# Kernel tuning notes

Measured on AMD Instinct MI355X. Metric: run time of the kernel, lower is better.

## Reference

```python
import jax, jax.numpy as jnp
import numpy as np

ALPHA = 1.0


def _bce_with_logits(x, y):
    # torch BCEWithLogitsLoss (mean): y*softplus(-x) + (1-y)*softplus(x)
    return jnp.mean(y * jax.nn.softplus(-x) + (1.0 - y) * jax.nn.softplus(x))


def _cross_entropy(logits, labels):
    # torch CrossEntropyLoss (mean) with int class labels
    logp = jax.nn.log_softmax(logits, axis=-1)
    return -jnp.mean(jnp.take_along_axis(logp, labels[:, None], axis=-1))


def setup_inputs() -> dict:
    key = jax.random.key(0)
    ks = jax.random.split(key, 6)
    B, T, C = 2097152, 4, 16
    return {
        "y_pred_binary": jax.random.normal(ks[0], (B,), dtype=jnp.float32),
        "y_pred_type": jax.random.normal(ks[1], (B, T), dtype=jnp.float32),
        "y_pred_source": jax.random.normal(ks[2], (B, C), dtype=jnp.float32),
        "y_true_binary": jnp.round(jax.random.uniform(ks[3], (B,), dtype=jnp.float32)),
        "y_true_type": jnp.round(jax.random.uniform(ks[4], (B, T), dtype=jnp.float32)),
        "y_true_source": jax.random.randint(ks[5], (B,), 0, C, dtype=jnp.int32),
    }


def reference(y_pred_binary, y_pred_type, y_pred_source,
              y_true_binary, y_true_type, y_true_source):
    loss = _bce_with_logits(y_pred_binary, y_true_binary)
    loss = loss + _bce_with_logits(y_pred_type, y_true_type)
    loss = loss + _cross_entropy(y_pred_source, y_true_source)

    # Non-differentiable consistency counts (torch computes these under
    # no_grad / via round+argmax, which carry no gradient).
    pb = jax.lax.stop_gradient(y_pred_binary)
    pt = jax.lax.stop_gradient(y_pred_type)
    ps = jax.lax.stop_gradient(y_pred_source)

    binary_c = jax.nn.sigmoid(pb) >= 0.5                     # [B] bool (round(sigmoid))
    type_c = jnp.any(jax.nn.sigmoid(pt) >= 0.5, axis=1)      # [B] bool
    source_c = jnp.argmax(ps, axis=1) > 0                    # [B] bool

    # XOR: exactly one of the pair active -> inconsistent
    cons_ab = jnp.mean((binary_c ^ type_c).astype(jnp.float32))
    cons_ac = jnp.mean((binary_c ^ source_c).astype(jnp.float32))

    loss = loss + ALPHA * cons_ab + ALPHA * cons_ac
    return loss
```

## Files before the change

kernel.cpp:

```cpp
#include <hip/hip_runtime.h>
#include <math.h>

#define CPB 4
#define ROWS_PER_BLOCK (256 * CPB)

__device__ __forceinline__ float fast_softplus(float x) {
    return fmaxf(x, 0.0f) + __logf(1.0f + __expf(-fabsf(x)));
}

struct Row {
    float  xb, yb;
    int    lab;
    float4 xt, yt;
    float4 r0, r1, r2, r3;
};

__device__ __forceinline__ Row load_row(const float* __restrict__ pb,
                                        const float* __restrict__ tb,
                                        const int*   __restrict__ ts,
                                        const float4* __restrict__ pt4,
                                        const float4* __restrict__ tt4,
                                        const float4* __restrict__ ps4,
                                        int row)
{
    Row R;
    R.xb  = pb[row];
    R.yb  = tb[row];
    R.lab = ts[row];
    R.xt  = pt4[row];
    R.yt  = tt4[row];
    size_t b = (size_t)row * 4;
    R.r0 = ps4[b + 0];
    R.r1 = ps4[b + 1];
    R.r2 = ps4[b + 2];
    R.r3 = ps4[b + 3];
    return R;
}

__device__ __forceinline__ float row_contrib(const Row& R)
{
    float c = fast_softplus(R.xb) - R.yb * R.xb;
    bool bin_c = (R.xb >= 0.0f);

    float tsum = (fast_softplus(R.xt.x) - R.yt.x * R.xt.x)
               + (fast_softplus(R.xt.y) - R.yt.y * R.xt.y)
               + (fast_softplus(R.xt.z) - R.yt.z * R.xt.z)
               + (fast_softplus(R.xt.w) - R.yt.w * R.xt.w);
    c += 0.25f * tsum;
    bool type_c = (R.xt.x >= 0.0f) || (R.xt.y >= 0.0f) ||
                  (R.xt.z >= 0.0f) || (R.xt.w >= 0.0f);

    float v[16] = { R.r0.x, R.r0.y, R.r0.z, R.r0.w,
                    R.r1.x, R.r1.y, R.r1.z, R.r1.w,
                    R.r2.x, R.r2.y, R.r2.z, R.r2.w,
                    R.r3.x, R.r3.y, R.r3.z, R.r3.w };
    float m = v[0];
    #pragma unroll
    for (int j = 1; j < 16; ++j) m = fmaxf(m, v[j]);
    float s = 0.0f;
    #pragma unroll
    for (int j = 0; j < 16; ++j) s += __expf(v[j] - m);
    float vlab = v[0];
    #pragma unroll
    for (int j = 1; j < 16; ++j) vlab = (R.lab == j) ? v[j] : vlab;
    c += m + __logf(s) - vlab;

    float mr = v[1];
    #pragma unroll
    for (int j = 2; j < 16; ++j) mr = fmaxf(mr, v[j]);
    bool src_c = (mr > v[0]);

    c += (bin_c != type_c) ? 1.0f : 0.0f;
    c += (bin_c != src_c)  ? 1.0f : 0.0f;
    return c;
}

__global__ __launch_bounds__(256, 2) void multitask_loss_kernel(
    const float*  __restrict__ pb,
    const float4* __restrict__ pt4,
    const float4* __restrict__ ps4,
    const float*  __restrict__ tb,
    const float4* __restrict__ tt4,
    const int*    __restrict__ ts,
    float*        __restrict__ partials)
{
    const int tid = threadIdx.x;
    const int row0 = blockIdx.x * ROWS_PER_BLOCK + tid;

    float acc = 0.0f;
    Row cur = load_row(pb, tb, ts, pt4, tt4, ps4, row0);
    #pragma unroll
    for (int i = 0; i < CPB - 1; ++i) {
        Row nxt = load_row(pb, tb, ts, pt4, tt4, ps4, row0 + (i + 1) * 256);
        acc += row_contrib(cur);
        cur = nxt;
    }
    acc += row_contrib(cur);

    #pragma unroll
    for (int off = 32; off > 0; off >>= 1)
        acc += __shfl_down(acc, off, 64);

    __shared__ float wsum[4];
    const int lane = tid & 63;
    const int wave = tid >> 6;
    if (lane == 0) wsum[wave] = acc;
    __syncthreads();
    if (tid == 0)
        partials[blockIdx.x] = wsum[0] + wsum[1] + wsum[2] + wsum[3];
}

__global__ __launch_bounds__(256) void reduce_kernel(
    const float* __restrict__ partials, int nblocks,
    const float*  __restrict__ pb,
    const float4* __restrict__ pt4,
    const float4* __restrict__ ps4,
    const float*  __restrict__ tb,
    const float4* __restrict__ tt4,
    const int*    __restrict__ ts,
    int n_main, int B,
    float* __restrict__ out, double invB)
{
    double s = 0.0;
    for (int i = threadIdx.x; i < nblocks; i += 256)
        s += (double)partials[i];
    for (int r = n_main + threadIdx.x; r < B; r += 256)
        s += (double)row_contrib(load_row(pb, tb, ts, pt4, tt4, ps4, r));

    #pragma unroll
    for (int off = 32; off > 0; off >>= 1)
        s += __shfl_down(s, off, 64);

    __shared__ double wsum[4];
    int lane = threadIdx.x & 63;
    int wave = threadIdx.x >> 6;
    if (lane == 0) wsum[wave] = s;
    __syncthreads();
    if (threadIdx.x == 0)
        out[0] = (float)((wsum[0] + wsum[1] + wsum[2] + wsum[3]) * invB);
}

extern "C" void kernel_launch(void* const* d_in, const int* in_sizes, int n_in,
                              void* d_out, int out_size, void* d_ws, size_t ws_size,
                              hipStream_t stream) {
    const float*  pb  = (const float*)d_in[0];
    const float4* pt4 = (const float4*)d_in[1];
    const float4* ps4 = (const float4*)d_in[2];
    const float*  tb  = (const float*)d_in[3];
    const float4* tt4 = (const float4*)d_in[4];
    const int*    ts  = (const int*)d_in[5];
    int B = in_sizes[0];

    float* partials = (float*)d_ws;

    int grid   = B / ROWS_PER_BLOCK;
    int n_main = grid * ROWS_PER_BLOCK;

    multitask_loss_kernel<<<grid, 256, 0, stream>>>(pb, pt4, ps4, tb, tt4, ts,
                                                    partials);
    reduce_kernel<<<1, 256, 0, stream>>>(partials, grid,
                                         pb, pt4, ps4, tb, tt4, ts,
                                         n_main, B, (float*)d_out,
                                         1.0 / (double)B);
}
```

Before: 265.9 us.

## Fold softplus/logsumexp logs into products, one row per thread, ballot penalties

```diff
diff --git a/kernel.cpp b/kernel.cpp
--- a/kernel.cpp
+++ b/kernel.cpp
@@ -1,110 +1,119 @@
 #include <hip/hip_runtime.h>
 #include <math.h>
 
-#define CPB 4
-#define ROWS_PER_BLOCK (256 * CPB)
+#define L2E 1.44269504088896340736f
+#define LN2 0.69314718055994530942f
 
-__device__ __forceinline__ float fast_softplus(float x) {
-    return fmaxf(x, 0.0f) + __logf(1.0f + __expf(-fabsf(x)));
-}
+#if __has_builtin(__builtin_amdgcn_exp2f)
+__device__ __forceinline__ float fexp2(float x)  { return __builtin_amdgcn_exp2f(x); }
+#else
+__device__ __forceinline__ float fexp2(float x)  { return __exp2f(x); }
+#endif
+#if __has_builtin(__builtin_amdgcn_logf)
+__device__ __forceinline__ float flog2(float x)  { return __builtin_amdgcn_logf(x); }
+#else
+__device__ __forceinline__ float flog2(float x)  { return __log2f(x); }
+#endif
 
-struct Row {
-    float  xb, yb;
-    int    lab;
-    float4 xt, yt;
-    float4 r0, r1, r2, r3;
-};
-
-__device__ __forceinline__ Row load_row(const float* __restrict__ pb,
-                                        const float* __restrict__ tb,
-                                        const int*   __restrict__ ts,
-                                        const float4* __restrict__ pt4,
-                                        const float4* __restrict__ tt4,
-                                        const float4* __restrict__ ps4,
-                                        int row)
+__device__ __forceinline__ float row_contrib_full(
+    const float* __restrict__ pb, const float4* __restrict__ pt4,
+    const float4* __restrict__ ps4, const float* __restrict__ tb,
+    const float4* __restrict__ tt4, const int* __restrict__ ts,
+    const float* __restrict__ psf, int row)
 {
-    Row R;
-    R.xb  = pb[row];
-    R.yb  = tb[row];
-    R.lab = ts[row];
-    R.xt  = pt4[row];
-    R.yt  = tt4[row];
+    float  xb = pb[row], yb = tb[row];
+    int    lab = ts[row];
+    float4 xt = pt4[row], yt = tt4[row];
     size_t b = (size_t)row * 4;
-    R.r0 = ps4[b + 0];
-    R.r1 = ps4[b + 1];
-    R.r2 = ps4[b + 2];
-    R.r3 = ps4[b + 3];
-    return R;
-}
-
-__device__ __forceinline__ float row_contrib(const Row& R)
-{
-    float c = fast_softplus(R.xb) - R.yb * R.xb;
-    bool bin_c = (R.xb >= 0.0f);
-
-    float tsum = (fast_softplus(R.xt.x) - R.yt.x * R.xt.x)
-               + (fast_softplus(R.xt.y) - R.yt.y * R.xt.y)
-               + (fast_softplus(R.xt.z) - R.yt.z * R.xt.z)
-               + (fast_softplus(R.xt.w) - R.yt.w * R.xt.w);
-    c += 0.25f * tsum;
-    bool type_c = (R.xt.x >= 0.0f) || (R.xt.y >= 0.0f) ||
-                  (R.xt.z >= 0.0f) || (R.xt.w >= 0.0f);
-
-    float v[16] = { R.r0.x, R.r0.y, R.r0.z, R.r0.w,
-                    R.r1.x, R.r1.y, R.r1.z, R.r1.w,
-                    R.r2.x, R.r2.y, R.r2.z, R.r2.w,
-                    R.r3.x, R.r3.y, R.r3.z, R.r3.w };
-    float m = v[0];
-    #pragma unroll
-    for (int j = 1; j < 16; ++j) m = fmaxf(m, v[j]);
+    float4 r0 = ps4[b+0], r1 = ps4[b+1], r2 = ps4[b+2], r3 = ps4[b+3];
+    float vlab = psf[(size_t)row * 16 + lab];
+    float v[16] = { r0.x,r0.y,r0.z,r0.w, r1.x,r1.y,r1.z,r1.w,
+                    r2.x,r2.y,r2.z,r2.w, r3.x,r3.y,r3.z,r3.w };
     float s = 0.0f;
-    #pragma unroll
-    for (int j = 0; j < 16; ++j) s += __expf(v[j] - m);
-    float vlab = v[0];
-    #pragma unroll
-    for (int j = 1; j < 16; ++j) vlab = (R.lab == j) ? v[j] : vlab;
-    c += m + __logf(s) - vlab;
-
+    for (int j = 0; j < 16; ++j) s += fexp2(v[j] * L2E);
+    float g = fexp2(xb * L2E);
+    float p = (1.0f+fexp2(xt.x*L2E))*(1.0f+fexp2(xt.y*L2E))
+            * (1.0f+fexp2(xt.z*L2E))*(1.0f+fexp2(xt.w*L2E));
+    float c = LN2 * (flog2(s * (1.0f+g)) + 0.25f * flog2(p));
+    float dot = xt.x*yt.x + xt.y*yt.y + xt.z*yt.z + xt.w*yt.w;
+    c = c - vlab - yb*xb - 0.25f*dot;
+    bool bin_c  = (xb >= 0.0f);
+    bool type_c = fmaxf(fmaxf(xt.x,xt.y), fmaxf(xt.z,xt.w)) >= 0.0f;
     float mr = v[1];
-    #pragma unroll
     for (int j = 2; j < 16; ++j) mr = fmaxf(mr, v[j]);
     bool src_c = (mr > v[0]);
-
     c += (bin_c != type_c) ? 1.0f : 0.0f;
     c += (bin_c != src_c)  ? 1.0f : 0.0f;
     return c;
 }
 
-__global__ __launch_bounds__(256, 2) void multitask_loss_kernel(
+__global__ __launch_bounds__(256) void multitask_loss_kernel(
     const float*  __restrict__ pb,
     const float4* __restrict__ pt4,
     const float4* __restrict__ ps4,
     const float*  __restrict__ tb,
     const float4* __restrict__ tt4,
     const int*    __restrict__ ts,
+    const float*  __restrict__ psf,
     float*        __restrict__ partials)
 {
     const int tid = threadIdx.x;
-    const int row0 = blockIdx.x * ROWS_PER_BLOCK + tid;
+    const int row = blockIdx.x * 256 + tid;
 
-    float acc = 0.0f;
-    Row cur = load_row(pb, tb, ts, pt4, tt4, ps4, row0);
+    float  xb = pb[row], yb = tb[row];
+    int    lab = ts[row];
+    float4 xt = pt4[row], yt = tt4[row];
+    size_t b = (size_t)row * 4;
+    float4 r0 = ps4[b+0], r1 = ps4[b+1], r2 = ps4[b+2], r3 = ps4[b+3];
+    float  vlab = psf[(size_t)row * 16 + lab];
+
+    float v[16] = { r0.x,r0.y,r0.z,r0.w, r1.x,r1.y,r1.z,r1.w,
+                    r2.x,r2.y,r2.z,r2.w, r3.x,r3.y,r3.z,r3.w };
+
+    float e[16];
     #pragma unroll
-    for (int i = 0; i < CPB - 1; ++i) {
-        Row nxt = load_row(pb, tb, ts, pt4, tt4, ps4, row0 + (i + 1) * 256);
-        acc += row_contrib(cur);
-        cur = nxt;
-    }
-    acc += row_contrib(cur);
+    for (int j = 0; j < 16; ++j) e[j] = fexp2(v[j] * L2E);
+    #pragma unroll
+    for (int st = 8; st >= 1; st >>= 1)
+        #pragma unroll
+        for (int j = 0; j < st; ++j) e[j] += e[j + st];
+    float s = e[0];
+
+    float g = fexp2(xb * L2E);
+    float s2 = s * (1.0f + g);
+
+    float f0 = fexp2(xt.x * L2E), f1 = fexp2(xt.y * L2E);
+    float f2 = fexp2(xt.z * L2E), f3 = fexp2(xt.w * L2E);
+    float p = ((1.0f+f0)*(1.0f+f1)) * ((1.0f+f2)*(1.0f+f3));
+
+    float c = LN2 * (flog2(s2) + 0.25f * flog2(p));
+
+    float dot = xt.x*yt.x + xt.y*yt.y + xt.z*yt.z + xt.w*yt.w;
+    c = c - vlab - yb*xb - 0.25f*dot;
+
+    bool bin_c  = (xb >= 0.0f);
+    bool type_c = fmaxf(fmaxf(xt.x, xt.y), fmaxf(xt.z, xt.w)) >= 0.0f;
+    float m01 = fmaxf(v[1],  v[2]),  m23 = fmaxf(v[3],  v[4]);
+    float m45 = fmaxf(v[5],  v[6]),  m67 = fmaxf(v[7],  v[8]);
+    float m89 = fmaxf(v[9],  v[10]), mab = fmaxf(v[11], v[12]);
+    float mcd = fmaxf(v[13], v[14]);
+    float mr  = fmaxf(fmaxf(fmaxf(m01, m23), fmaxf(m45, m67)),
+                      fmaxf(fmaxf(m89, mab), fmaxf(mcd, v[15])));
+    bool src_c = (mr > v[0]);
+
+    unsigned long long mb = __ballot(bin_c);
+    unsigned long long mt = __ballot(type_c);
+    unsigned long long ms = __ballot(src_c);
+    int pen = __popcll(mb ^ mt) + __popcll(mb ^ ms);
 
     #pragma unroll
     for (int off = 32; off > 0; off >>= 1)
-        acc += __shfl_down(acc, off, 64);
+        c += __shfl_down(c, off, 64);
 
     __shared__ float wsum[4];
     const int lane = tid & 63;
     const int wave = tid >> 6;
-    if (lane == 0) wsum[wave] = acc;
+    if (lane == 0) wsum[wave] = c + (float)pen;
     __syncthreads();
     if (tid == 0)
         partials[blockIdx.x] = wsum[0] + wsum[1] + wsum[2] + wsum[3];
@@ -112,20 +121,17 @@
 
 __global__ __launch_bounds__(256) void reduce_kernel(
     const float* __restrict__ partials, int nblocks,
-    const float*  __restrict__ pb,
-    const float4* __restrict__ pt4,
-    const float4* __restrict__ ps4,
-    const float*  __restrict__ tb,
-    const float4* __restrict__ tt4,
-    const int*    __restrict__ ts,
-    int n_main, int B,
-    float* __restrict__ out, double invB)
+    const float*  __restrict__ pb,  const float4* __restrict__ pt4,
+    const float4* __restrict__ ps4, const float*  __restrict__ tb,
+    const float4* __restrict__ tt4, const int*    __restrict__ ts,
+    const float*  __restrict__ psf,
+    int n_main, int B, float* __restrict__ out, double invB)
 {
     double s = 0.0;
     for (int i = threadIdx.x; i < nblocks; i += 256)
         s += (double)partials[i];
     for (int r = n_main + threadIdx.x; r < B; r += 256)
-        s += (double)row_contrib(load_row(pb, tb, ts, pt4, tt4, ps4, r));
+        s += (double)row_contrib_full(pb, pt4, ps4, tb, tt4, ts, psf, r);
 
     #pragma unroll
     for (int off = 32; off > 0; off >>= 1)
@@ -146,6 +152,7 @@
     const float*  pb  = (const float*)d_in[0];
     const float4* pt4 = (const float4*)d_in[1];
     const float4* ps4 = (const float4*)d_in[2];
+    const float*  psf = (const float*)d_in[2];
     const float*  tb  = (const float*)d_in[3];
     const float4* tt4 = (const float4*)d_in[4];
     const int*    ts  = (const int*)d_in[5];
@@ -153,13 +160,13 @@
 
     float* partials = (float*)d_ws;
 
-    int grid   = B / ROWS_PER_BLOCK;
-    int n_main = grid * ROWS_PER_BLOCK;
+    int grid   = B / 256;
+    int n_main = grid * 256;
 
     multitask_loss_kernel<<<grid, 256, 0, stream>>>(pb, pt4, ps4, tb, tt4, ts,
-                                                    partials);
+                                                    psf, partials);
     reduce_kernel<<<1, 256, 0, stream>>>(partials, grid,
-                                         pb, pt4, ps4, tb, tt4, ts,
+                                         pb, pt4, ps4, tb, tt4, ts, psf,
                                          n_main, B, (float*)d_out,
                                          1.0 / (double)B);
 }
```

New measurement: 262.6 us. Within noise of the previous version (-1.2%).
